# Performance work log

Measured on AMD Instinct MI355X. Metric: run time of the kernel, lower is better.

Reference implementation:

```python
import jax, jax.numpy as jnp
import numpy as np

N = 100000
E = 1600000
D_IN = 128   # point_feature_dim + scene_context_dim
H = 128
C = 8
EPS = 1e-5


def setup_inputs() -> dict:
    key = jax.random.key(0)
    ks = jax.random.split(key, 16)
    x = jax.random.normal(ks[0], (N, 64), dtype=jnp.float32)
    src = jax.random.randint(ks[1], (E,), 0, N, dtype=jnp.int32)
    dst = jax.random.randint(ks[2], (E,), 0, N, dtype=jnp.int32)
    scene_context = jax.random.normal(ks[3], (1, 64), dtype=jnp.float32)
    def lin(k, fan_in, fan_out):
        s = 1.0 / np.sqrt(fan_in)
        return jax.random.uniform(k, (fan_in, fan_out), jnp.float32, -s, s)
    W1 = lin(ks[4], D_IN, H); b1 = jnp.zeros((H,), jnp.float32)
    W2 = lin(ks[5], H, H);    b2 = jnp.zeros((H,), jnp.float32)
    g1 = jax.random.uniform(ks[6], (H,), jnp.float32, 0.5, 1.5)
    be1 = 0.1 * jax.random.normal(ks[7], (H,), jnp.float32)
    g2 = jax.random.uniform(ks[8], (H,), jnp.float32, 0.5, 1.5)
    be2 = 0.1 * jax.random.normal(ks[9], (H,), jnp.float32)
    Wout = lin(ks[10], H, C)
    bout = 0.01 * jax.random.normal(ks[11], (C,), jnp.float32)
    return {"x": x, "src": src, "dst": dst, "scene_context": scene_context,
            "W1": W1, "b1": b1, "g1": g1, "be1": be1,
            "W2": W2, "b2": b2, "g2": g2, "be2": be2,
            "Wout": Wout, "bout": bout}


def _gcn(h_in, W, b, src, dst, norm_edge, self_coef):
    # PyG GCNConv: linear transform, then symmetric-normalized aggregation
    # over edges plus self-loop, then bias.
    h = h_in @ W                                   # [N, H]
    msg = h[src] * norm_edge[:, None]              # gather + scale, [E, H]
    agg = jax.ops.segment_sum(msg, dst, num_segments=h.shape[0])
    return agg + h * self_coef[:, None] + b


def _bn(h, gamma, beta):
    mu = jnp.mean(h, axis=0)
    var = jnp.mean((h - mu) ** 2, axis=0)  # biased, training-mode BN
    return (h - mu) * jax.lax.rsqrt(var + EPS) * gamma + beta


def reference(x, src, dst, scene_context, W1, b1, g1, be1, W2, b2, g2, be2, Wout, bout):
    n = x.shape[0]
    # broadcast scene context to every node (batch=None branch)
    h = jnp.concatenate([x, jnp.broadcast_to(scene_context, (n, scene_context.shape[1]))], axis=-1)
    # degree with self-loops; symmetric normalization
    deg = jnp.ones((n,), x.dtype).at[dst].add(1.0)
    dinv = jax.lax.rsqrt(deg)
    norm_edge = dinv[src] * dinv[dst]              # [E]
    self_coef = dinv * dinv                        # [N]
    # block 1: GCN -> ReLU -> (dropout p=0) -> BN -> ReLU -> (dropout p=0)
    h = jax.nn.relu(_gcn(h, W1, b1, src, dst, norm_edge, self_coef))
    h = jax.nn.relu(_bn(h, g1, be1))
    # block 2
    h = jax.nn.relu(_gcn(h, W2, b2, src, dst, norm_edge, self_coef))
    h = jax.nn.relu(_bn(h, g2, be2))
    return h @ Wout + bout                         # [N, C]
```

## Files before the change

kernel.cpp:

```cpp
#include <hip/hip_runtime.h>
#include <math.h>

#define NN 100000
#define EE 1600000
#define HH 128
#define DX 64
#define CC 8
#define EPSV 1e-5f

#define NB 782
#define BCAP 4096
#define EPB 8192
#define NBLK_BIN ((EE + EPB - 1) / EPB)

typedef unsigned int u32;
typedef unsigned short u16;
typedef __attribute__((ext_vector_type(8))) short short8v;
typedef __attribute__((ext_vector_type(4))) float float4v;

__device__ __forceinline__ float bf2f(u16 h) {
    u32 u = ((u32)h) << 16;
    union { u32 u; float f; } c; c.u = u; return c.f;
}
__device__ __forceinline__ u16 f2b(float f) {
    union { float f; u32 u; } c; c.f = f;
    u32 r = (c.u + 0x7fffu + ((c.u >> 16) & 1u)) >> 16;
    return (u16)r;
}


__global__ void k_setup(const float* __restrict__ sctx,
                        const float* __restrict__ W1, const float* __restrict__ W2,
                        float* __restrict__ stats, int* __restrict__ btot,
                        int* __restrict__ gcursor,
                        float* __restrict__ cvec,
                        u16* __restrict__ Bt1, u16* __restrict__ Bt2) {
    int i = blockIdx.x * 256 + threadIdx.x;
    if (i < 512) stats[i] = 0.f;
    if (i < NB) { btot[i] = 0; gcursor[i] = i * BCAP; }
    if (i < 128 * 64) {
        int col = i >> 6, k = i & 63;
        Bt1[i] = f2b(W1[(size_t)k * HH + col]);
    } else if (i < 128 * 64 + 128 * 128) {
        int j = i - 128 * 64;
        int col = j >> 7, k = j & 127;
        Bt2[j] = f2b(W2[(size_t)k * HH + col]);
    }
    if (blockIdx.x == 96 && threadIdx.x < 128) {
        int f = threadIdx.x;
        float s = 0.f;
        #pragma unroll
        for (int j = 0; j < 64; ++j) s += sctx[j] * W1[(64 + j) * HH + f];
        cvec[f] = s;
    }
}

__global__ __launch_bounds__(1024) void k_bin(const int* __restrict__ src,
                                              const int* __restrict__ dst,
                                              int* __restrict__ btot,
                                              int* __restrict__ gcursor,
                                              u32* __restrict__ tmp) {
    __shared__ u32 rec[EPB];
    __shared__ int bcnt[NB], lstart[NB], gbase[NB], bofs[NB];
    __shared__ int part[1024];
    int t = threadIdx.x;
    int e0 = blockIdx.x * EPB;
    if (t < NB) { bcnt[t] = 0; bofs[t] = 0; }
    __syncthreads();
    int myd[8], mys[8];
    #pragma unroll
    for (int i = 0; i < 8; ++i) {
        int e = e0 + t + i * 1024;
        int d = -1, s = 0;
        if (e < EE) {
            d = dst[e]; s = src[e];
            atomicAdd(&bcnt[d >> 7], 1);
        }
        myd[i] = d; mys[i] = s;
    }
    __syncthreads();
    int c = (t < NB) ? bcnt[t] : 0;
    part[t] = c; __syncthreads();
    for (int d = 1; d < 1024; d <<= 1) {
        int x = (t >= d) ? part[t - d] : 0;
        __syncthreads();
        part[t] += x;
        __syncthreads();
    }
    if (t < NB) {
        lstart[t] = part[t] - c;
        if (c) {
            gbase[t] = atomicAdd(&gcursor[t], (c + 15) & ~15);
            atomicAdd(&btot[t], c);
        }
    }
    __syncthreads();
    #pragma unroll
    for (int i = 0; i < 8; ++i) {
        int d = myd[i];
        if (d >= 0) {
            int b = d >> 7;
            int lp = atomicAdd(&bofs[b], 1);
            rec[lstart[b] + lp] = (u32)mys[i] | ((u32)(d & 127) << 17);
        }
    }
    __syncthreads();
    int wv = t >> 6, ln = t & 63;
    for (int b = wv; b < NB; b += 16) {
        int n = bcnt[b];
        if (n) {
            int np = (n + 15) & ~15;
            int gb = gbase[b], ls = lstart[b];
            for (int j = ln; j < np; j += 64)
                tmp[gb + j] = (j < n) ? rec[ls + j] : 0xFFFFFFFFu;
        }
    }
}

__global__ void k_bscan(const int* __restrict__ btot, int* __restrict__ bbase) {
    __shared__ int ls[1024];
    int t = threadIdx.x;
    int v = (t < NB) ? btot[t] : 0;
    ls[t] = v; __syncthreads();
    for (int d = 1; d < 1024; d <<= 1) {
        int x = (t >= d) ? ls[t - d] : 0;
        __syncthreads();
        ls[t] += x;
        __syncthreads();
    }
    if (t < NB) bbase[t] = ls[t] - v;
}

__global__ __launch_bounds__(256) void k_csrA(const u32* __restrict__ tmp,
                                              const int* __restrict__ gcursor,
                                              const int* __restrict__ bbase,
                                              int* __restrict__ rowp,
                                              int* __restrict__ cnt,
                                              float* __restrict__ dinv) {
    __shared__ int lcnt[128];
    __shared__ int lofs[128];
    int b = blockIdx.x, t = threadIdx.x;
    if (t < 128) lcnt[t] = 0;
    __syncthreads();
    int beg = b * BCAP, end = gcursor[b];
    for (int i = beg + t; i < end; i += 256) {
        u32 r = tmp[i];
        if (r != 0xFFFFFFFFu) atomicAdd(&lcnt[(r >> 17) & 127], 1);
    }
    __syncthreads();
    int c = (t < 128) ? lcnt[t] : 0;
    if (t < 128) lofs[t] = c;
    __syncthreads();
    for (int d = 1; d < 128; d <<= 1) {
        int x = 0;
        if (t < 128 && t >= d) x = lofs[t - d];
        __syncthreads();
        if (t < 128) lofs[t] += x;
        __syncthreads();
    }
    if (t < 128) {
        int n = (b << 7) + t;
        if (n < NN) {
            rowp[n] = bbase[b] + lofs[t] - c;
            cnt[n] = c;
            dinv[n] = rsqrtf(1.0f + (float)c);
        }
    }
}

__global__ __launch_bounds__(256) void k_csrB(const u32* __restrict__ tmp,
                                              const int* __restrict__ gcursor,
                                              const int* __restrict__ rowp,
                                              const float* __restrict__ dinv,
                                              int2* __restrict__ ew) {
    __shared__ int lcur[128];
    __shared__ float ldin[128];
    int b = blockIdx.x, t = threadIdx.x;
    int n0 = b << 7;
    if (t < 128) {
        int n = n0 + t;
        lcur[t] = (n < NN) ? rowp[n] : 0;
        ldin[t] = (n < NN) ? dinv[n] : 0.f;
    }
    __syncthreads();
    int beg = b * BCAP;
    int end = gcursor[b];
    for (int i = beg + t; i < end; i += 256) {
        u32 r = tmp[i];
        if (r == 0xFFFFFFFFu) continue;
        int s = r & 0x1FFFF;
        int dl = (r >> 17) & 127;
        int pos = atomicAdd(&lcur[dl], 1);
        float w = dinv[s] * ldin[dl];
        ew[pos] = make_int2(s, __float_as_int(w));
    }
}


__global__ __launch_bounds__(256) void k_mgemm1(const float* __restrict__ x,
                                                const u16* __restrict__ Bt1,
                                                const float* __restrict__ cvec,
                                                u16* __restrict__ outp) {
    __shared__ u16 As[64 * 64];
    __shared__ u16 Bs[128 * 64];
    __shared__ float cvs[128];
    int t = threadIdx.x;
    int n0 = blockIdx.x * 64;
    if (t < 128) cvs[t] = cvec[t];

    #pragma unroll
    for (int l = 0; l < 4; ++l) {
        int idx = t + l * 256;
        int col = idx >> 3, kg = idx & 7;
        uint4 v = *(const uint4*)&Bt1[idx * 8];
        u32 byte = (u32)(col * 128 + kg * 16) ^ ((col & 7) << 4);
        *(uint4*)((char*)Bs + byte) = v;
    }
    #pragma unroll
    for (int l = 0; l < 4; ++l) {
        int idx = t + l * 256;
        int r = idx >> 4, fg = idx & 15;
        int n = n0 + r; if (n > NN - 1) n = NN - 1;
        float4 v = *(const float4*)&x[(size_t)n * DX + fg * 4];
        u32 lo = (u32)f2b(v.x) | ((u32)f2b(v.y) << 16);
        u32 hi = (u32)f2b(v.z) | ((u32)f2b(v.w) << 16);
        u32 byte = (u32)(r * 128 + fg * 8) ^ ((r & 7) << 4);
        *(uint2*)((char*)As + byte) = make_uint2(lo, hi);
    }
    __syncthreads();

    int w = t >> 6, lane = t & 63;
    int rl = lane & 15, kq = lane >> 4;
    int rbase = w * 16 + rl;
    float4v acc[8];
    #pragma unroll
    for (int nt = 0; nt < 8; ++nt) acc[nt] = (float4v){0.f, 0.f, 0.f, 0.f};

    #pragma unroll
    for (int kk = 0; kk < 2; ++kk) {
        u32 ab = (u32)(rbase * 128 + kk * 64 + kq * 16) ^ ((rbase & 7) << 4);
        short8v af = *(const short8v*)((const char*)As + ab);
        #pragma unroll
        for (int nt = 0; nt < 8; ++nt) {
            int col = nt * 16 + rl;
            u32 bb = (u32)(col * 128 + kk * 64 + kq * 16) ^ ((col & 7) << 4);
            short8v bf = *(const short8v*)((const char*)Bs + bb);
            acc[nt] = __builtin_amdgcn_mfma_f32_16x16x32_bf16(af, bf, acc[nt], 0, 0, 0);
        }
    }
    __syncthreads();
    #pragma unroll
    for (int nt = 0; nt < 8; ++nt) {
        int col = nt * 16 + rl;
        #pragma unroll
        for (int j = 0; j < 4; ++j) {
            int row = w * 16 + kq * 4 + j;
            u16 v = f2b(acc[nt][j] + cvs[col]);
            u32 byte = (u32)(row * 256 + col * 2) ^ ((row & 7) << 4);
            *(u16*)((char*)Bs + byte) = v;
        }
    }
    __syncthreads();
    #pragma unroll
    for (int l = 0; l < 4; ++l) {
        int idx = t + l * 256;
        int r = idx >> 4, kg = idx & 15;
        u32 byte = (u32)(r * 256 + kg * 16) ^ ((r & 7) << 4);
        uint4 v = *(const uint4*)((const char*)Bs + byte);
        int n = n0 + r;
        if (n < NN) *(uint4*)&outp[(size_t)n * HH + kg * 8] = v;
    }
}


__global__ __launch_bounds__(256) void k_mgemm2(const u16* __restrict__ hin,
                                                const u16* __restrict__ Bt2,
                                                const float* __restrict__ stats,
                                                const float* __restrict__ g,
                                                const float* __restrict__ be,
                                                u16* __restrict__ outp) {
    __shared__ u16 As[64 * 128];
    __shared__ u16 Bs[128 * 128];
    __shared__ float asc[128], csc[128];
    int t = threadIdx.x;
    int n0 = blockIdx.x * 64;
    if (t < 128) {
        float mu  = stats[t] * (1.0f / NN);
        float var = stats[128 + t] * (1.0f / NN) - mu * mu;
        float rs  = rsqrtf(var + EPSV);
        float a   = g[t] * rs;
        asc[t] = a;
        csc[t] = be[t] - mu * a;
    }
    #pragma unroll
    for (int l = 0; l < 8; ++l) {
        int idx = t + l * 256;
        int col = idx >> 4, kg = idx & 15;
        uint4 v = *(const uint4*)&Bt2[idx * 8];
        u32 byte = (u32)(col * 256 + kg * 16) ^ ((col & 7) << 4);
        *(uint4*)((char*)Bs + byte) = v;
    }
    __syncthreads();
    #pragma unroll
    for (int l = 0; l < 4; ++l) {
        int idx = t + l * 256;
        int r = idx >> 4, kg = idx & 15;
        int n = n0 + r; if (n > NN - 1) n = NN - 1;
        uint4 v = *(const uint4*)&hin[(size_t)n * HH + kg * 8];
        u32 wds[4] = {v.x, v.y, v.z, v.w};
        u32 pk[2][2];
        #pragma unroll
        for (int q = 0; q < 4; ++q) {
            int k = kg * 8 + q * 2;
            float x0 = bf2f((u16)(wds[q] & 0xffff));
            float x1 = bf2f((u16)(wds[q] >> 16));
            u16 o0 = f2b(fmaxf(fmaf(x0, asc[k],     csc[k]),     0.f));
            u16 o1 = f2b(fmaxf(fmaf(x1, asc[k + 1], csc[k + 1]), 0.f));
            pk[q >> 1][q & 1] = (u32)o0 | ((u32)o1 << 16);
        }
        uint4 ov = make_uint4(pk[0][0], pk[0][1], pk[1][0], pk[1][1]);
        u32 byte = (u32)(r * 256 + kg * 16) ^ ((r & 7) << 4);
        *(uint4*)((char*)As + byte) = ov;
    }
    __syncthreads();

    int w = t >> 6, lane = t & 63;
    int rl = lane & 15, kq = lane >> 4;
    int rbase = w * 16 + rl;
    float4v acc[8];
    #pragma unroll
    for (int nt = 0; nt < 8; ++nt) acc[nt] = (float4v){0.f, 0.f, 0.f, 0.f};

    #pragma unroll
    for (int kk = 0; kk < 4; ++kk) {
        u32 ab = (u32)(rbase * 256 + kk * 64 + kq * 16) ^ ((rbase & 7) << 4);
        short8v af = *(const short8v*)((const char*)As + ab);
        #pragma unroll
        for (int nt = 0; nt < 8; ++nt) {
            int col = nt * 16 + rl;
            u32 bb = (u32)(col * 256 + kk * 64 + kq * 16) ^ ((col & 7) << 4);
            short8v bf = *(const short8v*)((const char*)Bs + bb);
            acc[nt] = __builtin_amdgcn_mfma_f32_16x16x32_bf16(af, bf, acc[nt], 0, 0, 0);
        }
    }
    __syncthreads();
    #pragma unroll
    for (int nt = 0; nt < 8; ++nt) {
        int col = nt * 16 + rl;
        #pragma unroll
        for (int j = 0; j < 4; ++j) {
            int row = w * 16 + kq * 4 + j;
            u16 v = f2b(acc[nt][j]);
            u32 byte = (u32)(row * 256 + col * 2) ^ ((row & 7) << 4);
            *(u16*)((char*)As + byte) = v;
        }
    }
    __syncthreads();
    #pragma unroll
    for (int l = 0; l < 4; ++l) {
        int idx = t + l * 256;
        int r = idx >> 4, kg = idx & 15;
        u32 byte = (u32)(r * 256 + kg * 16) ^ ((r & 7) << 4);
        uint4 v = *(const uint4*)((const char*)As + byte);
        int n = n0 + r;
        if (n < NN) *(uint4*)&outp[(size_t)n * HH + kg * 8] = v;
    }
}


__global__ __launch_bounds__(256) void k_spmm(const u16* __restrict__ hlin,
                                              const int* __restrict__ rowp,
                                              const int* __restrict__ cnt,
                                              const int2* __restrict__ ew,
                                              const float* __restrict__ dinv,
                                              const float* __restrict__ b,
                                              u16* __restrict__ hout) {
    int wave = threadIdx.x >> 6;
    int lane = threadIdx.x & 63;
    int n = blockIdx.x * 4 + wave;
    int q = lane >> 4, li = lane & 15;
    int f0 = li * 8;
    float dn = dinv[n];
    float a[8];
    {
        uint4 r = *(const uint4*)&hlin[(size_t)n * HH + f0];
        float sc = (q == 0) ? dn * dn : 0.f;
        u32 wd[4] = {r.x, r.y, r.z, r.w};
        #pragma unroll
        for (int j = 0; j < 4; ++j) {
            a[j * 2 + 0] = sc * bf2f((u16)(wd[j] & 0xffff));
            a[j * 2 + 1] = sc * bf2f((u16)(wd[j] >> 16));
        }
    }
    int start = rowp[n], len = cnt[n];
    #pragma unroll 4
    for (int j = q; j < len; j += 4) {
        int2 e = ew[start + j];
        float wv = __int_as_float(e.y);
        uint4 r = *(const uint4*)&hlin[(size_t)e.x * HH + f0];
        u32 wd[4] = {r.x, r.y, r.z, r.w};
        #pragma unroll
        for (int k = 0; k < 4; ++k) {
            a[k * 2 + 0] = fmaf(bf2f((u16)(wd[k] & 0xffff)), wv, a[k * 2 + 0]);
            a[k * 2 + 1] = fmaf(bf2f((u16)(wd[k] >> 16)),    wv, a[k * 2 + 1]);
        }
    }
    #pragma unroll
    for (int k = 0; k < 8; ++k) {
        a[k] += __shfl_xor(a[k], 16);
        a[k] += __shfl_xor(a[k], 32);
    }
    if (q == 0) {
        float4 b0 = *(const float4*)&b[f0];
        float4 b1 = *(const float4*)&b[f0 + 4];
        float bb[8] = {b0.x, b0.y, b0.z, b0.w, b1.x, b1.y, b1.z, b1.w};
        u32 o[4];
        #pragma unroll
        for (int k = 0; k < 4; ++k) {
            float v0 = fmaxf(a[k * 2 + 0] + bb[k * 2 + 0], 0.f);
            float v1 = fmaxf(a[k * 2 + 1] + bb[k * 2 + 1], 0.f);
            o[k] = (u32)f2b(v0) | ((u32)f2b(v1) << 16);
        }
        uint4 pk = make_uint4(o[0], o[1], o[2], o[3]);
        *(uint4*)&hout[(size_t)n * HH + f0] = pk;
    }
}


__global__ __launch_bounds__(256) void k_stats(const u16* __restrict__ h,
                                               float* __restrict__ sums) {
    __shared__ float4 ls[4][64];
    int t = threadIdx.x;
    int lane = t & 63, wave = t >> 6;
    int f0 = lane * 2;
    float s0 = 0.f, s1 = 0.f, q0 = 0.f, q1 = 0.f;
    for (int row = blockIdx.x * 4 + wave; row < NN; row += gridDim.x * 4) {
        u32 v = *(const u32*)&h[(size_t)row * HH + f0];
        float a = bf2f((u16)(v & 0xffff));
        float c = bf2f((u16)(v >> 16));
        s0 += a; q0 += a * a;
        s1 += c; q1 += c * c;
    }
    ls[wave][lane] = make_float4(s0, s1, q0, q1);
    __syncthreads();
    if (wave == 0) {
        float4 r0 = ls[0][lane], r1 = ls[1][lane], r2 = ls[2][lane], r3 = ls[3][lane];
        atomicAdd(&sums[f0 + 0], r0.x + r1.x + r2.x + r3.x);
        atomicAdd(&sums[f0 + 1], r0.y + r1.y + r2.y + r3.y);
        atomicAdd(&sums[128 + f0 + 0], r0.z + r1.z + r2.z + r3.z);
        atomicAdd(&sums[128 + f0 + 1], r0.w + r1.w + r2.w + r3.w);
    }
}


__global__ __launch_bounds__(256) void k_out(const u16* __restrict__ h,
                                             const float* __restrict__ stats,
                                             const float* __restrict__ g,
                                             const float* __restrict__ be,
                                             const float* __restrict__ Wout,
                                             const float* __restrict__ bout,
                                             float* __restrict__ out) {
    __shared__ float hs[32][132];
    __shared__ float Wl[128][8];
    __shared__ float asc[128], csc[128];
    int t = threadIdx.x;
    if (t < 128) {
        float mu  = stats[256 + t] * (1.0f / NN);
        float var = stats[384 + t] * (1.0f / NN) - mu * mu;
        float rs  = rsqrtf(var + EPSV);
        float a   = g[t] * rs;
        asc[t] = a;
        csc[t] = be[t] - mu * a;
    }
    #pragma unroll
    for (int l = 0; l < 4; ++l) {
        int idx = t + l * 256;
        Wl[idx >> 3][idx & 7] = Wout[idx];
    }
    __syncthreads();

    int n0 = blockIdx.x * 32;
    #pragma unroll
    for (int l = 0; l < 2; ++l) {
        int idx = t + l * 256;
        int r = idx >> 4;
        int kg = idx & 15;
        uint4 v = *(const uint4*)&h[(size_t)(n0 + r) * HH + kg * 8];
        u32 w[4] = {v.x, v.y, v.z, v.w};
        int kk = kg * 8;
        #pragma unroll
        for (int qq = 0; qq < 4; ++qq) {
            float x0 = bf2f((u16)(w[qq] & 0xffff));
            float x1 = bf2f((u16)(w[qq] >> 16));
            hs[r][kk + qq * 2 + 0] = fmaxf(fmaf(x0, asc[kk + qq * 2 + 0], csc[kk + qq * 2 + 0]), 0.f);
            hs[r][kk + qq * 2 + 1] = fmaxf(fmaf(x1, asc[kk + qq * 2 + 1], csc[kk + qq * 2 + 1]), 0.f);
        }
    }
    __syncthreads();

    int c = t & 7, rl = t >> 3;
    float acc = 0.f;
    #pragma unroll 8
    for (int k = 0; k < 128; ++k) acc = fmaf(hs[rl][k], Wl[k][c], acc);
    out[(size_t)(n0 + rl) * CC + c] = acc + bout[c];
}


extern "C" void kernel_launch(void* const* d_in, const int* in_sizes, int n_in,
                              void* d_out, int out_size, void* d_ws, size_t ws_size,
                              hipStream_t stream) {
    const float* x    = (const float*)d_in[0];
    const int*   src  = (const int*)d_in[1];
    const int*   dst  = (const int*)d_in[2];
    const float* sctx = (const float*)d_in[3];
    const float* W1   = (const float*)d_in[4];
    const float* b1   = (const float*)d_in[5];
    const float* g1   = (const float*)d_in[6];
    const float* be1  = (const float*)d_in[7];
    const float* W2   = (const float*)d_in[8];
    const float* b2   = (const float*)d_in[9];
    const float* g2   = (const float*)d_in[10];
    const float* be2  = (const float*)d_in[11];
    const float* Wout = (const float*)d_in[12];
    const float* bout = (const float*)d_in[13];
    float* out = (float*)d_out;

    char* p = (char*)d_ws;
    auto carve = [&](size_t bytes) -> char* {
        char* r = p;
        p += (bytes + 255) & ~(size_t)255;
        return r;
    };
    u16*   hlin    = (u16*)carve((size_t)NN * HH * 2);
    u16*   hbuf    = (u16*)carve((size_t)NN * HH * 2);
    int2*  ew      = (int2*)carve((size_t)EE * 8 + 16);
    u32*   tmp     = (u32*)carve((size_t)NB * BCAP * 4 + 16);
    int*   cnt     = (int*)carve((size_t)NN * 4);
    int*   rowp    = (int*)carve((size_t)NN * 4);
    int*   gcursor = (int*)carve((size_t)NB * 4);
    int*   btot    = (int*)carve((size_t)NB * 4);
    int*   bbase   = (int*)carve((size_t)NB * 4);
    float* dinv    = (float*)carve((size_t)NN * 4);
    float* cvec    = (float*)carve(128 * 4);
    float* stats   = (float*)carve(512 * 4);
    u16*   Bt1     = (u16*)carve(128 * 64 * 2);
    u16*   Bt2     = (u16*)carve(128 * 128 * 2);

    k_setup<<<97, 256, 0, stream>>>(sctx, W1, W2, stats, btot, gcursor, cvec, Bt1, Bt2);
    k_bin<<<NBLK_BIN, 1024, 0, stream>>>(src, dst, btot, gcursor, tmp);
    k_bscan<<<1, 1024, 0, stream>>>(btot, bbase);
    k_csrA<<<NB, 256, 0, stream>>>(tmp, gcursor, bbase, rowp, cnt, dinv);
    k_csrB<<<NB, 256, 0, stream>>>(tmp, gcursor, rowp, dinv, ew);

    k_mgemm1<<<(NN + 63) / 64, 256, 0, stream>>>(x, Bt1, cvec, hlin);
    k_spmm<<<NN / 4, 256, 0, stream>>>(hlin, rowp, cnt, ew, dinv, b1, hbuf);
    k_stats<<<512, 256, 0, stream>>>(hbuf, stats);
    k_mgemm2<<<(NN + 63) / 64, 256, 0, stream>>>(hbuf, Bt2, stats, g1, be1, hlin);
    k_spmm<<<NN / 4, 256, 0, stream>>>(hlin, rowp, cnt, ew, dinv, b2, hbuf);
    k_stats<<<512, 256, 0, stream>>>(hbuf, stats + 256);
    k_out<<<NN / 32, 256, 0, stream>>>(hbuf, stats, g2, be2, Wout, bout, out);
}
```

Measured before the change: 305.7 us.

## Aggregate raw 64-dim features before first GCN matmul, fold scene context via row sums

Reorders the first GCN layer as (A·X)·W instead of A·(X·W), so the sparse aggregation gathers 64-dim bf16 node features instead of 128-dim transformed ones. The constant scene-context term is folded in through a per-node sum of normalized edge weights, computed in the CSR build, times the precomputed context vector. Bias and ReLU move into the GEMM epilogue. It adds an x-to-bf16 conversion pass in setup and an extra rounding of the aggregated features to bf16 before the matmul.

Result: faster. 296.8 us (-2.9%).

```diff
diff --git a/kernel.cpp b/kernel.cpp
--- a/kernel.cpp
+++ b/kernel.cpp
@@ -31,10 +31,12 @@
 
 __global__ void k_setup(const float* __restrict__ sctx,
                         const float* __restrict__ W1, const float* __restrict__ W2,
+                        const float* __restrict__ x,
                         float* __restrict__ stats, int* __restrict__ btot,
                         int* __restrict__ gcursor,
                         float* __restrict__ cvec,
-                        u16* __restrict__ Bt1, u16* __restrict__ Bt2) {
+                        u16* __restrict__ Bt1, u16* __restrict__ Bt2,
+                        u16* __restrict__ xb) {
     int i = blockIdx.x * 256 + threadIdx.x;
     if (i < 512) stats[i] = 0.f;
     if (i < NB) { btot[i] = 0; gcursor[i] = i * BCAP; }
@@ -52,6 +54,13 @@
         #pragma unroll
         for (int j = 0; j < 64; ++j) s += sctx[j] * W1[(64 + j) * HH + f];
         cvec[f] = s;
+    }
+    if (i < NN * (DX / 4)) {
+        float4 v = ((const float4*)x)[i];
+        uint2 pk;
+        pk.x = (u32)f2b(v.x) | ((u32)f2b(v.y) << 16);
+        pk.y = (u32)f2b(v.z) | ((u32)f2b(v.w) << 16);
+        ((uint2*)xb)[i] = pk;
     }
 }
 
@@ -82,9 +91,9 @@
     int c = (t < NB) ? bcnt[t] : 0;
     part[t] = c; __syncthreads();
     for (int d = 1; d < 1024; d <<= 1) {
-        int x = (t >= d) ? part[t - d] : 0;
+        int xk = (t >= d) ? part[t - d] : 0;
         __syncthreads();
-        part[t] += x;
+        part[t] += xk;
         __syncthreads();
     }
     if (t < NB) {
@@ -172,15 +181,19 @@
                                               const int* __restrict__ gcursor,
                                               const int* __restrict__ rowp,
                                               const float* __restrict__ dinv,
-                                              int2* __restrict__ ew) {
+                                              int2* __restrict__ ew,
+                                              float* __restrict__ rowsum) {
     __shared__ int lcur[128];
     __shared__ float ldin[128];
+    __shared__ float lsum[128];
     int b = blockIdx.x, t = threadIdx.x;
     int n0 = b << 7;
     if (t < 128) {
         int n = n0 + t;
         lcur[t] = (n < NN) ? rowp[n] : 0;
-        ldin[t] = (n < NN) ? dinv[n] : 0.f;
+        float dv = (n < NN) ? dinv[n] : 0.f;
+        ldin[t] = dv;
+        lsum[t] = dv * dv;
     }
     __syncthreads();
     int beg = b * BCAP;
@@ -193,20 +206,78 @@
         int pos = atomicAdd(&lcur[dl], 1);
         float w = dinv[s] * ldin[dl];
         ew[pos] = make_int2(s, __float_as_int(w));
-    }
-}
-
-
-__global__ __launch_bounds__(256) void k_mgemm1(const float* __restrict__ x,
+        atomicAdd(&lsum[dl], w);
+    }
+    __syncthreads();
+    if (t < 128) {
+        int n = n0 + t;
+        if (n < NN) rowsum[n] = lsum[t];
+    }
+}
+
+
+__global__ __launch_bounds__(256) void k_spmm1(const u16* __restrict__ xb,
+                                               const int* __restrict__ rowp,
+                                               const int* __restrict__ cnt,
+                                               const int2* __restrict__ ew,
+                                               const float* __restrict__ dinv,
+                                               u16* __restrict__ xp) {
+    int wave = threadIdx.x >> 6;
+    int lane = threadIdx.x & 63;
+    int n = blockIdx.x * 4 + wave;
+    int q = lane >> 4, li = lane & 15;
+    int f0 = li * 4;
+    float dn = dinv[n];
+    float a[4];
+    {
+        uint2 r = *(const uint2*)&xb[(size_t)n * DX + f0];
+        float sc = (q == 0) ? dn * dn : 0.f;
+        a[0] = sc * bf2f((u16)(r.x & 0xffff));
+        a[1] = sc * bf2f((u16)(r.x >> 16));
+        a[2] = sc * bf2f((u16)(r.y & 0xffff));
+        a[3] = sc * bf2f((u16)(r.y >> 16));
+    }
+    int start = rowp[n], len = cnt[n];
+    #pragma unroll 4
+    for (int j = q; j < len; j += 4) {
+        int2 e = ew[start + j];
+        float wv = __int_as_float(e.y);
+        uint2 r = *(const uint2*)&xb[(size_t)e.x * DX + f0];
+        a[0] = fmaf(bf2f((u16)(r.x & 0xffff)), wv, a[0]);
+        a[1] = fmaf(bf2f((u16)(r.x >> 16)),    wv, a[1]);
+        a[2] = fmaf(bf2f((u16)(r.y & 0xffff)), wv, a[2]);
+        a[3] = fmaf(bf2f((u16)(r.y >> 16)),    wv, a[3]);
+    }
+    #pragma unroll
+    for (int k = 0; k < 4; ++k) {
+        a[k] += __shfl_xor(a[k], 16);
+        a[k] += __shfl_xor(a[k], 32);
+    }
+    if (q == 0) {
+        uint2 pk;
+        pk.x = (u32)f2b(a[0]) | ((u32)f2b(a[1]) << 16);
+        pk.y = (u32)f2b(a[2]) | ((u32)f2b(a[3]) << 16);
+        *(uint2*)&xp[(size_t)n * DX + f0] = pk;
+    }
+}
+
+
+__global__ __launch_bounds__(256) void k_mgemm1(const u16* __restrict__ xp,
                                                 const u16* __restrict__ Bt1,
                                                 const float* __restrict__ cvec,
+                                                const float* __restrict__ b1,
+                                                const float* __restrict__ rowsum,
                                                 u16* __restrict__ outp) {
     __shared__ u16 As[64 * 64];
     __shared__ u16 Bs[128 * 64];
-    __shared__ float cvs[128];
+    __shared__ float cvs[128], bs[128], rsum[64];
     int t = threadIdx.x;
     int n0 = blockIdx.x * 64;
-    if (t < 128) cvs[t] = cvec[t];
+    if (t < 128) { cvs[t] = cvec[t]; bs[t] = b1[t]; }
+    if (t < 64) {
+        int n = n0 + t;
+        rsum[t] = (n < NN) ? rowsum[n] : 0.f;
+    }
 
     #pragma unroll
     for (int l = 0; l < 4; ++l) {
@@ -217,15 +288,13 @@
         *(uint4*)((char*)Bs + byte) = v;
     }
     #pragma unroll
-    for (int l = 0; l < 4; ++l) {
-        int idx = t + l * 256;
-        int r = idx >> 4, fg = idx & 15;
+    for (int l = 0; l < 2; ++l) {
+        int idx = t + l * 256;
+        int r = idx >> 3, kg = idx & 7;
         int n = n0 + r; if (n > NN - 1) n = NN - 1;
-        float4 v = *(const float4*)&x[(size_t)n * DX + fg * 4];
-        u32 lo = (u32)f2b(v.x) | ((u32)f2b(v.y) << 16);
-        u32 hi = (u32)f2b(v.z) | ((u32)f2b(v.w) << 16);
-        u32 byte = (u32)(r * 128 + fg * 8) ^ ((r & 7) << 4);
-        *(uint2*)((char*)As + byte) = make_uint2(lo, hi);
+        uint4 v = *(const uint4*)&xp[(size_t)n * DX + kg * 8];
+        u32 byte = (u32)(r * 128 + kg * 16) ^ ((r & 7) << 4);
+        *(uint4*)((char*)As + byte) = v;
     }
     __syncthreads();
 
@@ -255,7 +324,8 @@
         #pragma unroll
         for (int j = 0; j < 4; ++j) {
             int row = w * 16 + kq * 4 + j;
-            u16 v = f2b(acc[nt][j] + cvs[col]);
+            float o = acc[nt][j] + rsum[row] * cvs[col] + bs[col];
+            u16 v = f2b(fmaxf(o, 0.f));
             u32 byte = (u32)(row * 256 + col * 2) ^ ((row & 7) << 4);
             *(u16*)((char*)Bs + byte) = v;
         }
@@ -533,6 +603,8 @@
     };
     u16*   hlin    = (u16*)carve((size_t)NN * HH * 2);
     u16*   hbuf    = (u16*)carve((size_t)NN * HH * 2);
+    u16*   xb      = (u16*)carve((size_t)NN * DX * 2);
+    u16*   xp      = (u16*)carve((size_t)NN * DX * 2);
     int2*  ew      = (int2*)carve((size_t)EE * 8 + 16);
     u32*   tmp     = (u32*)carve((size_t)NB * BCAP * 4 + 16);
     int*   cnt     = (int*)carve((size_t)NN * 4);
@@ -541,19 +613,21 @@
     int*   btot    = (int*)carve((size_t)NB * 4);
     int*   bbase   = (int*)carve((size_t)NB * 4);
     float* dinv    = (float*)carve((size_t)NN * 4);
+    float* rowsum  = (float*)carve((size_t)NN * 4);
     float* cvec    = (float*)carve(128 * 4);
     float* stats   = (float*)carve(512 * 4);
     u16*   Bt1     = (u16*)carve(128 * 64 * 2);
     u16*   Bt2     = (u16*)carve(128 * 128 * 2);
 
-    k_setup<<<97, 256, 0, stream>>>(sctx, W1, W2, stats, btot, gcursor, cvec, Bt1, Bt2);
+    k_setup<<<(NN * (DX / 4) + 255) / 256, 256, 0, stream>>>(
+        sctx, W1, W2, x, stats, btot, gcursor, cvec, Bt1, Bt2, xb);
     k_bin<<<NBLK_BIN, 1024, 0, stream>>>(src, dst, btot, gcursor, tmp);
     k_bscan<<<1, 1024, 0, stream>>>(btot, bbase);
     k_csrA<<<NB, 256, 0, stream>>>(tmp, gcursor, bbase, rowp, cnt, dinv);
-    k_csrB<<<NB, 256, 0, stream>>>(tmp, gcursor, rowp, dinv, ew);
-
-    k_mgemm1<<<(NN + 63) / 64, 256, 0, stream>>>(x, Bt1, cvec, hlin);
-    k_spmm<<<NN / 4, 256, 0, stream>>>(hlin, rowp, cnt, ew, dinv, b1, hbuf);
+    k_csrB<<<NB, 256, 0, stream>>>(tmp, gcursor, rowp, dinv, ew, rowsum);
+
+    k_spmm1<<<NN / 4, 256, 0, stream>>>(xb, rowp, cnt, ew, dinv, xp);
+    k_mgemm1<<<(NN + 63) / 64, 256, 0, stream>>>(xp, Bt1, cvec, b1, rowsum, hbuf);
     k_stats<<<512, 256, 0, stream>>>(hbuf, stats);
     k_mgemm2<<<(NN + 63) / 64, 256, 0, stream>>>(hbuf, Bt2, stats, g1, be1, hlin);
     k_spmm<<<NN / 4, 256, 0, stream>>>(hlin, rowp, cnt, ew, dinv, b2, hbuf);
```
